# Kernel optimization log

Measured on AMD Instinct MI355X. Metric: run time of the kernel, lower is better.

## Reference

```python
import jax, jax.numpy as jnp
import numpy as np

B, L, D, NHEAD, NLAYERS = 2, 2048, 256, 8, 8
NAMES = ['self', 'cross'] * 4


def setup_inputs() -> dict:
    key = jax.random.key(0)
    ks = jax.random.split(key, 6)
    w_scale = D ** -0.5  # keep activations well-scaled
    return {
        'f0': jax.random.normal(ks[0], (B, L, D), dtype=jnp.float32),
        'f1': jax.random.normal(ks[1], (B, L, D), dtype=jnp.float32),
        'Wq': jax.random.normal(ks[2], (NLAYERS, D, D), dtype=jnp.float32) * w_scale,
        'Wk': jax.random.normal(ks[3], (NLAYERS, D, D), dtype=jnp.float32) * w_scale,
        'Wv': jax.random.normal(ks[4], (NLAYERS, D, D), dtype=jnp.float32) * w_scale,
        'Wo': jax.random.normal(ks[5], (NLAYERS, D, D), dtype=jnp.float32) * w_scale,
    }


def _rope(x, inv_freq):
    # x: (B, L, D); RoPE over the FULL model dim (matches original, mixes heads)
    L_, D_ = x.shape[1], x.shape[2]
    t = jnp.arange(L_, dtype=jnp.float32)
    freqs = t[:, None] * inv_freq[None, :]          # (L, D/2)
    emb = jnp.concatenate([freqs, freqs], axis=-1)  # (L, D)
    x1, x2 = x[..., : D_ // 2], x[..., D_ // 2:]
    rot = jnp.concatenate([-x2, x1], axis=-1)
    return x * jnp.cos(emb) + rot * jnp.sin(emb)


def _attn(x, src, wq, wk, wv, wo, use_rope, inv_freq):
    b, l1, d = x.shape
    l2 = src.shape[1]
    dh = d // NHEAD
    q = x @ wq.T    # torch Linear: x @ W^T
    k = src @ wk.T
    v = src @ wv.T
    if use_rope:
        q = _rope(q, inv_freq)
        k = _rope(k, inv_freq)
    q = q.reshape(b, l1, NHEAD, dh)
    k = k.reshape(b, l2, NHEAD, dh)
    v = v.reshape(b, l2, NHEAD, dh)
    scores = jnp.einsum('bqhd,bkhd->bhqk', q, k) * (dh ** -0.5)
    out = jnp.einsum('bhqk,bkhd->bqhd', jax.nn.softmax(scores, axis=-1), v)
    return out.reshape(b, l1, d) @ wo.T


def reference(f0, f1, Wq, Wk, Wv, Wo):
    d = f0.shape[-1]
    inv_freq = 1.0 / (10000.0 ** (jnp.arange(0, d, 2, dtype=jnp.float32) / d))
    for i, name in enumerate(NAMES):
        if name == 'self':
            f0 = f0 + _attn(f0, f0, Wq[i], Wk[i], Wv[i], Wo[i], True, inv_freq)
            f1 = f1 + _attn(f1, f1, Wq[i], Wk[i], Wv[i], Wo[i], True, inv_freq)
        else:
            # sequential updates: second cross uses the UPDATED f0 (matches torch)
            f0 = f0 + _attn(f0, f1, Wq[i], Wk[i], Wv[i], Wo[i], False, inv_freq)
            f1 = f1 + _attn(f1, f0, Wq[i], Wk[i], Wv[i], Wo[i], False, inv_freq)
    return (f0, f1)
```

## Files before the change

### kernel.cpp

```cpp
#include <hip/hip_runtime.h>

#define BB   2
#define LL   2048
#define DD   256
#define NH   8
#define MM   (BB*LL)
#define NLAYERS 8
#define MMDD ((size_t)MM*DD)

typedef unsigned short ushort_t;
typedef __attribute__((ext_vector_type(8))) short  short8;
typedef __attribute__((ext_vector_type(4))) float  f32x4;
typedef __attribute__((ext_vector_type(4))) unsigned int u32x4;
typedef __attribute__((ext_vector_type(2))) unsigned int u32x2;

#define CSC 0.2550500394f

#define WAITV0 asm volatile("s_waitcnt vmcnt(0)" ::: "memory")
#define WAITV2 asm volatile("s_waitcnt vmcnt(2)" ::: "memory")
#define WAITV4 asm volatile("s_waitcnt vmcnt(4)" ::: "memory")
#define WAITV6 asm volatile("s_waitcnt vmcnt(6)" ::: "memory")
#define WAITLG asm volatile("s_waitcnt lgkmcnt(0)" ::: "memory")
#define BAR()  __builtin_amdgcn_s_barrier()
#define SCHED0 __builtin_amdgcn_sched_barrier(0)

__device__ __forceinline__ f32x4 mfma16(short8 a, short8 b, f32x4 c) {
    return __builtin_amdgcn_mfma_f32_16x16x32_bf16(a, b, c, 0, 0, 0);
}
__device__ __forceinline__ unsigned cvtpk(float lo, float hi) {
    unsigned r;
    asm volatile("v_cvt_pk_bf16_f32 %0, %1, %2" : "=v"(r) : "v"(lo), "v"(hi));
    return r;
}
__device__ __forceinline__ void pl32(unsigned &a, unsigned &b) {
    asm volatile("v_permlane32_swap_b32 %0, %1" : "+v"(a), "+v"(b));
}
__device__ __forceinline__ float bf2f(unsigned short h) {
    return __builtin_bit_cast(float, ((unsigned)h) << 16);
}
__device__ __forceinline__ void gll16(const void* gsrc, void* ldst) {
    __builtin_amdgcn_global_load_lds(
        (const __attribute__((address_space(1))) unsigned int*)gsrc,
        (__attribute__((address_space(3))) unsigned int*)ldst, 16, 0, 0);
}


__global__ __launch_bounds__(256) void setup(const float* __restrict__ f0,
                                             const float* __restrict__ f1,
                                             const float* __restrict__ Wq,
                                             const float* __restrict__ Wk,
                                             const float* __restrict__ Wv,
                                             const float* __restrict__ Wo,
                                             float* __restrict__ F,
                                             ushort_t* __restrict__ Fb,
                                             ushort_t* __restrict__ Wb,
                                             float* __restrict__ tab) {
    int b = blockIdx.x, t = threadIdx.x;
    if (b < 1024) {
        int i = b * 256 + t;
        const float* src = (i < 131072) ? f0 : f1;
        int loc = i & 131071;
        const f32x4* p = (const f32x4*)(src + (size_t)loc * 8);
        f32x4 a = p[0], bb = p[1];
        *(f32x4*)&F[(size_t)i * 8]     = a;
        *(f32x4*)&F[(size_t)i * 8 + 4] = bb;
        u32x4 o = {cvtpk(a.x, a.y), cvtpk(a.z, a.w), cvtpk(bb.x, bb.y), cvtpk(bb.z, bb.w)};
        *(u32x4*)&Fb[(size_t)i * 8] = o;
    } else if (b < 2048) {
        int i = (b - 1024) * 256 + t;
        int reg = i >> 16, loc = i & 65535;
        const float* src = reg == 0 ? Wq : reg == 1 ? Wk : reg == 2 ? Wv : Wo;
        const f32x4* p = (const f32x4*)(src + (size_t)loc * 8);
        f32x4 x = p[0], y = p[1];
        u32x4 o = {cvtpk(x.x, x.y), cvtpk(x.z, x.w), cvtpk(y.x, y.y), cvtpk(y.z, y.w)};
        *(u32x4*)&Wb[(size_t)reg * 524288 + (size_t)loc * 8] = o;
    } else {
        int idx = (b - 2048) * 256 + t;
        int p = idx >> 7, j = idx & 127;
        float inv = __expf(-((float)j / 128.f) * 9.210340371976184f);
        float s, c;
        sincosf((float)p * inv, &s, &c);
        tab[(size_t)p * 256 + j]       = c;
        tab[(size_t)p * 256 + 128 + j] = s;
    }
}

__global__ __launch_bounds__(256) void gemmQK(const ushort_t* __restrict__ X,
                                              const ushort_t* __restrict__ WQ,
                                              const ushort_t* __restrict__ WK,
                                              ushort_t* __restrict__ DQ,
                                              ushort_t* __restrict__ KT,
                                              const float* __restrict__ tab) {
    __shared__ ushort_t Xb[2][4096];
    __shared__ ushort_t WbL[2][4096];
    __shared__ ushort_t WbH[2][4096];
    const int tid = threadIdx.x, ln = tid & 63, w = tid >> 6;
    const int f = blockIdx.x;
    const int xcd = f & 7, u = f >> 3;
    const int bx = u & 3, byg = u >> 2;
    const int mat = bx >> 1, cg = bx & 1;
    const int by = xcd * 16 + byg;
    const int m0 = by * 64, n0 = cg * 64;
    const ushort_t* W = mat ? WK : WQ;

    auto stage = [&](int c, int buf) {
#pragma unroll
        for (int i = 0; i < 2; i++) {
            int sl = (w * 2 + i) * 64 + ln;
            int r = sl >> 3, x = sl & 7;
            int col = c * 64 + ((x ^ (r & 7)) << 3);
            gll16(X + (size_t)(m0 + r) * 256 + col,       &Xb[buf][(w * 2 + i) * 512]);
            gll16(W + (size_t)(n0 + r) * 256 + col,       &WbL[buf][(w * 2 + i) * 512]);
            gll16(W + (size_t)(n0 + 128 + r) * 256 + col, &WbH[buf][(w * 2 + i) * 512]);
        }
    };

    const int ql = ln & 15, gq = ln >> 4;
    const int wm = w >> 1, wn = w & 1;
    f32x4 z4 = {0.f, 0.f, 0.f, 0.f};
    f32x4 accL[2][2] = {{z4, z4}, {z4, z4}};
    f32x4 accH[2][2] = {{z4, z4}, {z4, z4}};

    stage(0, 0);
    stage(1, 1);
#pragma unroll
    for (int c = 0; c < 4; c++) {
        if (c < 3) { WAITV6; } else { WAITV0; }
        BAR(); SCHED0;
        const ushort_t* XL = Xb[c & 1];
        const ushort_t* WL = WbL[c & 1];
        const ushort_t* WH = WbH[c & 1];
        __builtin_amdgcn_s_setprio(1);
#pragma unroll
        for (int ks = 0; ks < 2; ks++) {
            int cc = ks * 4 + gq;
            int r0 = 32 * wm + ql, r1 = r0 + 16;
            int nr0 = 32 * wn + ql, nr1 = nr0 + 16;
            short8 a0 = *(const short8*)&XL[(r0 * 8 + (cc ^ (r0 & 7))) * 8];
            short8 a1 = *(const short8*)&XL[(r1 * 8 + (cc ^ (r1 & 7))) * 8];
            short8 l0 = *(const short8*)&WL[(nr0 * 8 + (cc ^ (nr0 & 7))) * 8];
            short8 l1 = *(const short8*)&WL[(nr1 * 8 + (cc ^ (nr1 & 7))) * 8];
            short8 h0 = *(const short8*)&WH[(nr0 * 8 + (cc ^ (nr0 & 7))) * 8];
            short8 h1 = *(const short8*)&WH[(nr1 * 8 + (cc ^ (nr1 & 7))) * 8];
            accL[0][0] = mfma16(a0, l0, accL[0][0]);
            accL[0][1] = mfma16(a0, l1, accL[0][1]);
            accL[1][0] = mfma16(a1, l0, accL[1][0]);
            accL[1][1] = mfma16(a1, l1, accL[1][1]);
            accH[0][0] = mfma16(a0, h0, accH[0][0]);
            accH[0][1] = mfma16(a0, h1, accH[0][1]);
            accH[1][0] = mfma16(a1, h0, accH[1][0]);
            accH[1][1] = mfma16(a1, h1, accH[1][1]);
        }
        __builtin_amdgcn_s_setprio(0);
        BAR();
        if (c + 2 < 4) stage(c + 2, c & 1);
    }

#pragma unroll
    for (int mf = 0; mf < 2; mf++)
#pragma unroll
        for (int nf = 0; nf < 2; nf++)
#pragma unroll
            for (int r = 0; r < 4; r++) {
                int mg = m0 + 32 * wm + 16 * mf + gq * 4 + r;
                int jl = n0 + 32 * wn + 16 * nf + ql;
                int pos = mg & (LL - 1);
                float a = accL[mf][nf][r], b = accH[mf][nf][r];
                float c = tab[(size_t)pos * 256 + jl];
                float s = tab[(size_t)pos * 256 + 128 + jl];
                float o1 = a * c - b * s;
                float o2 = b * c + a * s;
                if (mat == 0) {
                    o1 *= CSC; o2 *= CSC;
                    DQ[(size_t)mg * 256 + jl]       = (ushort_t)cvtpk(o1, o1);
                    DQ[(size_t)mg * 256 + jl + 128] = (ushort_t)cvtpk(o2, o2);
                } else {
                    int z = mg >> 11, key = mg & 2047;
                    int tt = key >> 6, kk = key & 63;
                    int dh = jl & 31, hA = jl >> 5;
                    size_t base = (size_t)tt * 2048 + (size_t)(dh >> 3) * 512
                                + (size_t)kk * 8 + (dh & 7);
                    KT[(size_t)(z * 8 + hA) * 65536 + base]     = (ushort_t)cvtpk(o1, o1);
                    KT[(size_t)(z * 8 + hA + 4) * 65536 + base] = (ushort_t)cvtpk(o2, o2);
                }
            }
}

template<int NQ, int NK, int NV, int QMODE, int KMODE, int NTY>
__global__ __launch_bounds__(256) void gemm5(const ushort_t* __restrict__ X,
                                             const ushort_t* __restrict__ WQ,
                                             const ushort_t* __restrict__ WK,
                                             const ushort_t* __restrict__ WV,
                                             ushort_t* __restrict__ DQ,
                                             ushort_t* __restrict__ DK,
                                             ushort_t* __restrict__ DVT) {
    constexpr int NTX = NQ + NK + NV;
    __shared__ ushort_t Xb[3][4096];
    __shared__ ushort_t Wb[3][4096];
    const int tid = threadIdx.x, ln = tid & 63, w = tid >> 6;
    const int f = blockIdx.x;
    const int xcd = f & 7, s = f >> 3;
    const int bx = s % NTX, byg = s / NTX;
    const int by = xcd * (NTY / 8) + byg;
    const int m0 = by * 64;

    const ushort_t* W; ushort_t* DH; int n0, mode;
    if (NQ && bx < NQ)           { W = WQ; DH = DQ;  mode = QMODE; n0 = bx * 64; }
    else if (NK && bx < NQ + NK) { W = WK; DH = DK;  mode = KMODE; n0 = (bx - NQ) * 64; }
    else                         { W = WV; DH = DVT; mode = 3; n0 = (bx - NQ - NK) * 64; }

    auto stage = [&](int c, int buf) {
#pragma unroll
        for (int i = 0; i < 2; i++) {
            int sl = (w * 2 + i) * 64 + ln;
            int r = sl >> 3, x = sl & 7;
            int col = c * 64 + ((x ^ (r & 7)) << 3);
            gll16(X + (size_t)(m0 + r) * 256 + col, &Xb[buf][(w * 2 + i) * 512]);
            gll16(W + (size_t)(n0 + r) * 256 + col, &Wb[buf][(w * 2 + i) * 512]);
        }
    };

    const int ql = ln & 15, gq = ln >> 4;
    const int wm = w >> 1, wn = w & 1;
    f32x4 z4 = {0.f, 0.f, 0.f, 0.f};
    f32x4 acc[2][2] = {{z4, z4}, {z4, z4}};

    stage(0, 0);
    stage(1, 1);
#pragma unroll
    for (int c = 0; c < 4; c++) {
        if (c < 3) { WAITV4; } else { WAITV0; }
        BAR(); SCHED0;
        if (c + 2 < 4) stage(c + 2, (c + 2) % 3);
        const ushort_t* XL = Xb[c % 3];
        const ushort_t* WL = Wb[c % 3];
        __builtin_amdgcn_s_setprio(1);
#pragma unroll
        for (int ks = 0; ks < 2; ks++) {
            int cc = ks * 4 + gq;
            int r0 = 32 * wm + ql, r1 = r0 + 16;
            int nr0 = 32 * wn + ql, nr1 = nr0 + 16;
            short8 a0 = *(const short8*)&XL[(r0 * 8 + (cc ^ (r0 & 7))) * 8];
            short8 a1 = *(const short8*)&XL[(r1 * 8 + (cc ^ (r1 & 7))) * 8];
            short8 b0 = *(const short8*)&WL[(nr0 * 8 + (cc ^ (nr0 & 7))) * 8];
            short8 b1 = *(const short8*)&WL[(nr1 * 8 + (cc ^ (nr1 & 7))) * 8];
            acc[0][0] = mfma16(a0, b0, acc[0][0]);
            acc[0][1] = mfma16(a0, b1, acc[0][1]);
            acc[1][0] = mfma16(a1, b0, acc[1][0]);
            acc[1][1] = mfma16(a1, b1, acc[1][1]);
        }
        __builtin_amdgcn_s_setprio(0);
    }

    if (mode == 3) {
        float* scr = (float*)&Xb[0][0];
        __syncthreads();
#pragma unroll
        for (int mf = 0; mf < 2; mf++)
#pragma unroll
            for (int nf = 0; nf < 2; nf++)
#pragma unroll
                for (int r = 0; r < 4; r++) {
                    int nloc = 32 * wn + 16 * nf + ql;
                    int mloc = 32 * wm + 16 * mf + 4 * gq + r;
                    scr[nloc * 65 + mloc] = acc[mf][nf][r];
                }
        __syncthreads();
        int nloc = tid >> 2, mc = (tid & 3) * 16;
        int ng = n0 + nloc, hh = ng >> 5, dh = ng & 31;
        int mg = m0 + mc;
        int z = mg >> 11, key = mg & 2047;
        int tt = key >> 6;
        int ks = (mc >> 5) & 1, J = (mc >> 4) & 1;
        int cA = 4 * ks + 2 * J, cB = cA + 1;
        int swz = dh & 7;
        const float* sc = &scr[nloc * 65 + mc];
        u32x2 q0 = {cvtpk(sc[0], sc[1]),   cvtpk(sc[2], sc[3])};
        u32x2 q1 = {cvtpk(sc[4], sc[5]),   cvtpk(sc[6], sc[7])};
        u32x2 q2 = {cvtpk(sc[8], sc[9]),   cvtpk(sc[10], sc[11])};
        u32x2 q3 = {cvtpk(sc[12], sc[13]), cvtpk(sc[14], sc[15])};
        ushort_t* base = &DVT[(size_t)(z * 8 + hh) * 65536 + (size_t)tt * 2048 + dh * 64];
        *(u32x2*)&base[(cA ^ swz) * 8]     = q0;
        *(u32x2*)&base[(cB ^ swz) * 8]     = q1;
        *(u32x2*)&base[(cA ^ swz) * 8 + 4] = q2;
        *(u32x2*)&base[(cB ^ swz) * 8 + 4] = q3;
    } else {
#pragma unroll
        for (int mf = 0; mf < 2; mf++)
#pragma unroll
            for (int nf = 0; nf < 2; nf++)
#pragma unroll
                for (int r = 0; r < 4; r++) {
                    int mg = m0 + 32 * wm + 16 * mf + gq * 4 + r;
                    int ng = n0 + 32 * wn + 16 * nf + ql;
                    float v = acc[mf][nf][r];
                    if (mode == 2) {
                        DH[(size_t)mg * 256 + ng] = (ushort_t)cvtpk(v, v);
                    } else if (mode == 5) {
                        int zh = (mg >> 11) * 8 + (ng >> 5);
                        size_t off = (size_t)zh * 65536
                                   + (size_t)((mg & 2047) >> 6) * 2048
                                   + (size_t)((ng & 31) >> 3) * 512
                                   + (size_t)(mg & 63) * 8 + (ng & 7);
                        DH[off] = (ushort_t)cvtpk(v, v);
                    } else {
                        float vs = v * CSC;
                        DH[(size_t)mg * 256 + ng] = (ushort_t)cvtpk(vs, vs);
                    }
                }
    }
}

template<int SPLIT, int NTY>
__global__ __launch_bounds__(256) void gemmO(const ushort_t* __restrict__ Opb,
                                             const float* __restrict__ Lp,
                                             const ushort_t* __restrict__ W,
                                             const float* __restrict__ Res,
                                             float* __restrict__ OutF,
                                             ushort_t* __restrict__ OutH,
                                             int mrows) {
    __shared__ ushort_t Xf[64 * 256];
    __shared__ ushort_t Wpb[3][4096];
    const int tid = threadIdx.x, ln = tid & 63, w = tid >> 6;
    const int f = blockIdx.x;
    const int xcd = f & 7, s = f >> 3;
    const int bx = s & 3, byg = s >> 2;
    const int by = xcd * (NTY / 8) + byg;
    const int m0 = by * 64, n0 = bx * 64;

    auto stageW = [&](int c, int buf) {
#pragma unroll
        for (int i = 0; i < 2; i++) {
            int sl = (w * 2 + i) * 64 + ln;
            int r = sl >> 3, x = sl & 7;
            int col = c * 64 + ((x ^ (r & 7)) << 3);
            gll16(W + (size_t)(n0 + r) * 256 + col, &Wpb[buf][(w * 2 + i) * 512]);
        }
    };
    stageW(0, 0);
    stageW(1, 1);

    const int xr = tid >> 2, q = tid & 3, hb = q >> 1;
    float inv[4];
#pragma unroll
    for (int hh = 0; hh < 4; hh++) {
        float l = 0.f;
#pragma unroll
        for (int sp = 0; sp < SPLIT; sp++)
            l += Lp[(size_t)sp * mrows * 8 + (size_t)(m0 + xr) * 8 + 2 * hh + hb];
        inv[hh] = 1.f / l;
    }
#pragma unroll
    for (int p = 0; p < 4; p++) {
        int col = q * 16 + 64 * p;
        f32x4 a0 = {0.f,0.f,0.f,0.f}, a1 = a0, a2 = a0, a3 = a0;
#pragma unroll
        for (int sp = 0; sp < SPLIT; sp++) {
            const ushort_t* src = &Opb[((size_t)sp * mrows + m0 + xr) * 256 + col];
            u32x4 v0 = *(const u32x4*)&src[0];
            u32x4 v1 = *(const u32x4*)&src[8];
            f32x4 b0 = {bf2f(v0.x & 0xffff), bf2f(v0.x >> 16),
                        bf2f(v0.y & 0xffff), bf2f(v0.y >> 16)};
            f32x4 b1 = {bf2f(v0.z & 0xffff), bf2f(v0.z >> 16),
                        bf2f(v0.w & 0xffff), bf2f(v0.w >> 16)};
            f32x4 b2 = {bf2f(v1.x & 0xffff), bf2f(v1.x >> 16),
                        bf2f(v1.y & 0xffff), bf2f(v1.y >> 16)};
            f32x4 b3 = {bf2f(v1.z & 0xffff), bf2f(v1.z >> 16),
                        bf2f(v1.w & 0xffff), bf2f(v1.w >> 16)};
            a0 += b0; a1 += b1; a2 += b2; a3 += b3;
        }
        float iv = inv[p];
        a0 *= iv; a1 *= iv; a2 *= iv; a3 *= iv;
        u32x4 w0 = {cvtpk(a0.x, a0.y), cvtpk(a0.z, a0.w),
                    cvtpk(a1.x, a1.y), cvtpk(a1.z, a1.w)};
        u32x4 w1 = {cvtpk(a2.x, a2.y), cvtpk(a2.z, a2.w),
                    cvtpk(a3.x, a3.y), cvtpk(a3.z, a3.w)};
        int xc0 = q * 2;
        *(u32x4*)&Xf[xr * 256 + p * 64 + ((xc0)     ^ (xr & 7)) * 8] = w0;
        *(u32x4*)&Xf[xr * 256 + p * 64 + ((xc0 + 1) ^ (xr & 7)) * 8] = w1;
    }
    WAITLG;
    BAR(); SCHED0;

    const int ql = ln & 15, gq = ln >> 4;
    const int wm = w >> 1, wn = w & 1;
    f32x4 z4 = {0.f, 0.f, 0.f, 0.f};
    f32x4 acc[2][2] = {{z4, z4}, {z4, z4}};
#pragma unroll
    for (int c = 0; c < 4; c++) {
        if (c < 3) { WAITV2; } else { WAITV0; }
        BAR(); SCHED0;
        if (c + 2 < 4) stageW(c + 2, (c + 2) % 3);
        const ushort_t* WL = Wpb[c % 3];
        __builtin_amdgcn_s_setprio(1);
#pragma unroll
        for (int ks = 0; ks < 2; ks++) {
            int cc = ks * 4 + gq;
            int r0 = 32 * wm + ql, r1 = r0 + 16;
            int nr0 = 32 * wn + ql, nr1 = nr0 + 16;
            short8 a0 = *(const short8*)&Xf[r0 * 256 + c * 64 + (cc ^ (r0 & 7)) * 8];
            short8 a1 = *(const short8*)&Xf[r1 * 256 + c * 64 + (cc ^ (r1 & 7)) * 8];
            short8 b0 = *(const short8*)&WL[(nr0 * 8 + (cc ^ (nr0 & 7))) * 8];
            short8 b1 = *(const short8*)&WL[(nr1 * 8 + (cc ^ (nr1 & 7))) * 8];
            acc[0][0] = mfma16(a0, b0, acc[0][0]);
            acc[0][1] = mfma16(a0, b1, acc[0][1]);
            acc[1][0] = mfma16(a1, b0, acc[1][0]);
            acc[1][1] = mfma16(a1, b1, acc[1][1]);
        }
        __builtin_amdgcn_s_setprio(0);
    }

#pragma unroll
    for (int mf = 0; mf < 2; mf++)
#pragma unroll
        for (int nf = 0; nf < 2; nf++)
#pragma unroll
            for (int r = 0; r < 4; r++) {
                int mg = m0 + 32 * wm + 16 * mf + gq * 4 + r;
                int ng = n0 + 32 * wn + 16 * nf + ql;
                size_t idx = (size_t)mg * 256 + ng;
                float o = Res[idx] + acc[mf][nf][r];
                OutF[idx] = o;
                OutH[idx] = (ushort_t)cvtpk(o, o);
            }
}

template<int SPLIT>
__global__ __launch_bounds__(256, 6) void attn10(const ushort_t* __restrict__ Q,
                                                 const ushort_t* __restrict__ K,
                                                 const ushort_t* __restrict__ Vt,
                                                 ushort_t* __restrict__ Opb,
                                                 float* __restrict__ Lp, int mrows) {
    __shared__ ushort_t K_lds[3][2048];
    __shared__ ushort_t V_lds[3][2048];

    const int tid = threadIdx.x, ln = tid & 63, w = tid >> 6;
    const int ql = ln & 15, gq = ln >> 4;
    const int f = blockIdx.x;
    const int xcd = f & 7, slot = f >> 3;
    const int qb = slot & 15, gg = slot >> 4;
    const int h = xcd;
    const int zz = gg / SPLIT, sp = gg % SPLIT;
    const int t0 = (sp * 32) / SPLIT;
    const int NT = ((sp + 1) * 32) / SPLIT - t0;
    const int q0 = qb * 128 + w * 32;
    const size_t rb = (size_t)zz * 2048;
    const int zh = zz * 8 + h;

    short8 qfA = *(const short8*)&Q[(rb + q0 + ql) * 256 + h * 32 + gq * 8];
    short8 qfB = *(const short8*)&Q[(rb + q0 + 16 + ql) * 256 + h * 32 + gq * 8];

    const ushort_t* kt = K  + (size_t)zh * 65536 + (size_t)t0 * 2048 + tid * 8;
    const ushort_t* vt = Vt + (size_t)zh * 65536 + (size_t)t0 * 2048 + tid * 8;

    gll16(kt,        &K_lds[0][w * 512]);
    gll16(vt,        &V_lds[0][w * 512]);
    gll16(kt + 2048, &K_lds[1][w * 512]);
    gll16(vt + 2048, &V_lds[1][w * 512]);

    const short os = (short)0x3F80;
    const short8 ones = {os, os, os, os, os, os, os, os};
    f32x4 z4 = {0.f, 0.f, 0.f, 0.f};
    f32x4 o0A = z4, o1A = z4, o0B = z4, o1B = z4, laccA = z4, laccB = z4;

    int cur = 0, pre = 2;
    for (int t = 0; t < NT; t++) {
        if (t < NT - 1) { WAITV2; } else { WAITV0; }
        BAR(); SCHED0;
        if (t + 2 < NT) {
            gll16(kt + (size_t)(t + 2) * 2048, &K_lds[pre][w * 512]);
            gll16(vt + (size_t)(t + 2) * 2048, &V_lds[pre][w * 512]);
        }
        const ushort_t* KL = K_lds[cur];
        const ushort_t* VL = V_lds[cur];

        f32x4 stA[4], stB[4];
        __builtin_amdgcn_s_setprio(1);
#pragma unroll
        for (int j = 0; j < 4; j++) {
            short8 kf = *(const short8*)&KL[(gq * 64 + 16 * j + ql) * 8];
            stA[j] = mfma16(kf, qfA, z4);
            stB[j] = mfma16(kf, qfB, z4);
        }
        __builtin_amdgcn_s_setprio(0);
#pragma unroll
        for (int j = 0; j < 4; j++)
#pragma unroll
            for (int r = 0; r < 4; r++) {
                stA[j][r] = __builtin_amdgcn_exp2f(stA[j][r]);
                stB[j][r] = __builtin_amdgcn_exp2f(stB[j][r]);
            }
        unsigned aLo[4], aHi[4], bLo[4], bHi[4];
#pragma unroll
        for (int j = 0; j < 4; j++) {
            aLo[j] = cvtpk(stA[j][0], stA[j][1]);
            aHi[j] = cvtpk(stA[j][2], stA[j][3]);
            bLo[j] = cvtpk(stB[j][0], stB[j][1]);
            bHi[j] = cvtpk(stB[j][2], stB[j][3]);
        }
        pl32(aLo[0], aLo[1]); pl32(aHi[0], aHi[1]);
        pl32(aLo[2], aLo[3]); pl32(aHi[2], aHi[3]);
        pl32(bLo[0], bLo[1]); pl32(bHi[0], bHi[1]);
        pl32(bLo[2], bLo[3]); pl32(bHi[2], bHi[3]);
        u32x4 fA0 = {aLo[0], aHi[0], aLo[1], aHi[1]};
        u32x4 fA1 = {aLo[2], aHi[2], aLo[3], aHi[3]};
        u32x4 fB0 = {bLo[0], bHi[0], bLo[1], bHi[1]};
        u32x4 fB1 = {bLo[2], bHi[2], bLo[3], bHi[3]};
        short8 pfA0 = __builtin_bit_cast(short8, fA0);
        short8 pfA1 = __builtin_bit_cast(short8, fA1);
        short8 pfB0 = __builtin_bit_cast(short8, fB0);
        short8 pfB1 = __builtin_bit_cast(short8, fB1);

        __builtin_amdgcn_s_setprio(1);
#pragma unroll
        for (int ks = 0; ks < 2; ks++) {
            int sw = (4 * ks + gq) ^ (ql & 7);
            short8 vf0 = *(const short8*)&VL[(ql * 8 + sw) * 8];
            short8 vf1 = *(const short8*)&VL[((16 + ql) * 8 + sw) * 8];
            short8 pA = ks ? pfA1 : pfA0;
            short8 pB = ks ? pfB1 : pfB0;
            o0A = mfma16(vf0, pA, o0A);
            o1A = mfma16(vf1, pA, o1A);
            o0B = mfma16(vf0, pB, o0B);
            o1B = mfma16(vf1, pB, o1B);
            laccA = mfma16(ones, pA, laccA);
            laccB = mfma16(ones, pB, laccB);
        }
        __builtin_amdgcn_s_setprio(0);
        cur = (cur == 2) ? 0 : cur + 1;
        pre = (pre == 2) ? 0 : pre + 1;
    }

    size_t rowA = rb + q0 + ql, rowB = rowA + 16;
    ushort_t* obA = Opb + ((size_t)sp * mrows + rowA) * 256 + h * 32;
    ushort_t* obB = Opb + ((size_t)sp * mrows + rowB) * 256 + h * 32;
    u32x2 wA0 = {cvtpk(o0A.x, o0A.y), cvtpk(o0A.z, o0A.w)};
    u32x2 wA1 = {cvtpk(o1A.x, o1A.y), cvtpk(o1A.z, o1A.w)};
    u32x2 wB0 = {cvtpk(o0B.x, o0B.y), cvtpk(o0B.z, o0B.w)};
    u32x2 wB1 = {cvtpk(o1B.x, o1B.y), cvtpk(o1B.z, o1B.w)};
    *(u32x2*)&obA[gq * 4]      = wA0;
    *(u32x2*)&obA[16 + gq * 4] = wA1;
    *(u32x2*)&obB[gq * 4]      = wB0;
    *(u32x2*)&obB[16 + gq * 4] = wB1;
    if (gq == 0) {
        Lp[(size_t)sp * mrows * 8 + rowA * 8 + h] = laccA[0];
        Lp[(size_t)sp * mrows * 8 + rowB * 8 + h] = laccB[0];
    }
}

extern "C" void kernel_launch(void* const* d_in, const int* in_sizes, int n_in,
                              void* d_out, int out_size, void* d_ws, size_t ws_size,
                              hipStream_t stream) {
    const float* f0_in = (const float*)d_in[0];
    const float* f1_in = (const float*)d_in[1];
    const float* Wq = (const float*)d_in[2];
    const float* Wk = (const float*)d_in[3];
    const float* Wv = (const float*)d_in[4];
    const float* Wo = (const float*)d_in[5];

    float* F0 = (float*)d_out;
    float* F1 = F0 + MMDD;

    ushort_t* Fb  = (ushort_t*)d_ws;
    ushort_t* Qb  = Fb  + 2 * MMDD;
    ushort_t* Khb = Qb  + 2 * MMDD;
    ushort_t* Vhb = Khb + 2 * MMDD;
    ushort_t* Wb  = Vhb + 2 * MMDD;
    ushort_t* Opb = Wb  + 2 * MMDD;
    float*    Lpw = (float*)(Opb + 8 * MMDD);
    float*    tab = Lpw + 262144;

    ushort_t* Wqb = Wb;
    ushort_t* Wkb = Wb + (size_t)NLAYERS * 65536;
    ushort_t* Wvb = Wb + (size_t)2 * NLAYERS * 65536;
    ushort_t* Wob = Wb + (size_t)3 * NLAYERS * 65536;

    setup<<<3072, 256, 0, stream>>>(f0_in, f1_in, Wq, Wk, Wv, Wo, F0, Fb, Wb, tab);

    for (int i = 0; i < NLAYERS; i++) {
        const ushort_t* wq = Wqb + (size_t)i * 65536;
        const ushort_t* wk = Wkb + (size_t)i * 65536;
        const ushort_t* wv = Wvb + (size_t)i * 65536;
        const ushort_t* wo = Wob + (size_t)i * 65536;

        if ((i & 1) == 0) {
            gemmQK<<<512, 256, 0, stream>>>(Fb, wq, wk, Qb, Khb, tab);
            gemm5<0, 0, 4, 0, 0, 128><<<512, 256, 0, stream>>>(
                Fb, nullptr, nullptr, wv, nullptr, nullptr, Vhb);
            attn10<3><<<1536, 256, 0, stream>>>(Qb, Khb, Vhb, Opb, Lpw, MM * 2);
            gemmO<3, 128><<<512, 256, 0, stream>>>(Opb, Lpw, wo, F0, F0, Fb, MM * 2);
        } else {
            gemm5<4, 0, 0, 4, 0, 128><<<512, 256, 0, stream>>>(
                Fb, wq, nullptr, nullptr, Qb, nullptr, nullptr);
            for (int s = 0; s < 2; s++) {
                const ushort_t* sb = Fb + (size_t)(1 - s) * MMDD;
                float* xf = s ? F1 : F0;
                ushort_t* xbw = Fb + (size_t)s * MMDD;
                gemm5<0, 4, 4, 0, 5, 64><<<512, 256, 0, stream>>>(
                    sb, nullptr, wk, wv, nullptr, Khb, Vhb);
                attn10<8><<<2048, 256, 0, stream>>>(Qb + (size_t)s * MMDD,
                                                    Khb, Vhb, Opb, Lpw, MM);
                gemmO<8, 64><<<256, 256, 0, stream>>>(Opb, Lpw, wo, xf, xf, xbw, MM);
            }
        }
    }
}
```

Measured before the change: 513.5 us.

## Merge QKV projection launches and slim the attention kernel's pipeline and row-sum

The separate Q/K and V projection kernels are merged into one launch for self layers, and the Q and first K/V projection are merged for cross layers, cutting launch count and tail idle time. The attention kernel goes from triple to double buffering of K/V tiles with a full vmcnt wait, raises its occupancy hint to 8 blocks, and splits self-attention four ways instead of three. The softmax denominator is now summed in scalar registers with a cross-lane shuffle at the end, replacing the extra MFMA against a ones vector. The trade-off is less load/compute overlap in attention, exposing memory latency more, in exchange for higher occupancy and less matrix work.

```diff
diff --git a/kernel.cpp b/kernel.cpp
--- a/kernel.cpp
+++ b/kernel.cpp
@@ -85,17 +85,14 @@
     }
 }
 
-__global__ __launch_bounds__(256) void gemmQK(const ushort_t* __restrict__ X,
-                                              const ushort_t* __restrict__ WQ,
-                                              const ushort_t* __restrict__ WK,
-                                              ushort_t* __restrict__ DQ,
-                                              ushort_t* __restrict__ KT,
-                                              const float* __restrict__ tab) {
-    __shared__ ushort_t Xb[2][4096];
-    __shared__ ushort_t WbL[2][4096];
-    __shared__ ushort_t WbH[2][4096];
+__device__ __forceinline__ void gemmQK_body(int f, ushort_t* lds,
+                                            const ushort_t* __restrict__ X,
+                                            const ushort_t* __restrict__ WQ,
+                                            const ushort_t* __restrict__ WK,
+                                            ushort_t* __restrict__ DQ,
+                                            ushort_t* __restrict__ KT,
+                                            const float* __restrict__ tab) {
     const int tid = threadIdx.x, ln = tid & 63, w = tid >> 6;
-    const int f = blockIdx.x;
     const int xcd = f & 7, u = f >> 3;
     const int bx = u & 3, byg = u >> 2;
     const int mat = bx >> 1, cg = bx & 1;
@@ -109,9 +106,9 @@
             int sl = (w * 2 + i) * 64 + ln;
             int r = sl >> 3, x = sl & 7;
             int col = c * 64 + ((x ^ (r & 7)) << 3);
-            gll16(X + (size_t)(m0 + r) * 256 + col,       &Xb[buf][(w * 2 + i) * 512]);
-            gll16(W + (size_t)(n0 + r) * 256 + col,       &WbL[buf][(w * 2 + i) * 512]);
-            gll16(W + (size_t)(n0 + 128 + r) * 256 + col, &WbH[buf][(w * 2 + i) * 512]);
+            gll16(X + (size_t)(m0 + r) * 256 + col,       &lds[buf * 4096 + (w * 2 + i) * 512]);
+            gll16(W + (size_t)(n0 + r) * 256 + col,       &lds[8192 + buf * 4096 + (w * 2 + i) * 512]);
+            gll16(W + (size_t)(n0 + 128 + r) * 256 + col, &lds[16384 + buf * 4096 + (w * 2 + i) * 512]);
         }
     };
 
@@ -127,9 +124,9 @@
     for (int c = 0; c < 4; c++) {
         if (c < 3) { WAITV6; } else { WAITV0; }
         BAR(); SCHED0;
-        const ushort_t* XL = Xb[c & 1];
-        const ushort_t* WL = WbL[c & 1];
-        const ushort_t* WH = WbH[c & 1];
+        const ushort_t* XL = &lds[(c & 1) * 4096];
+        const ushort_t* WL = &lds[8192 + (c & 1) * 4096];
+        const ushort_t* WH = &lds[16384 + (c & 1) * 4096];
         __builtin_amdgcn_s_setprio(1);
 #pragma unroll
         for (int ks = 0; ks < 2; ks++) {
@@ -187,18 +184,16 @@
 }
 
 template<int NQ, int NK, int NV, int QMODE, int KMODE, int NTY>
-__global__ __launch_bounds__(256) void gemm5(const ushort_t* __restrict__ X,
-                                             const ushort_t* __restrict__ WQ,
-                                             const ushort_t* __restrict__ WK,
-                                             const ushort_t* __restrict__ WV,
-                                             ushort_t* __restrict__ DQ,
-                                             ushort_t* __restrict__ DK,
-                                             ushort_t* __restrict__ DVT) {
+__device__ __forceinline__ void gemm5_body(int f, ushort_t* lds,
+                                           const ushort_t* __restrict__ X,
+                                           const ushort_t* __restrict__ WQ,
+                                           const ushort_t* __restrict__ WK,
+                                           const ushort_t* __restrict__ WV,
+                                           ushort_t* __restrict__ DQ,
+                                           ushort_t* __restrict__ DK,
+                                           ushort_t* __restrict__ DVT) {
     constexpr int NTX = NQ + NK + NV;
-    __shared__ ushort_t Xb[3][4096];
-    __shared__ ushort_t Wb[3][4096];
     const int tid = threadIdx.x, ln = tid & 63, w = tid >> 6;
-    const int f = blockIdx.x;
     const int xcd = f & 7, s = f >> 3;
     const int bx = s % NTX, byg = s / NTX;
     const int by = xcd * (NTY / 8) + byg;
@@ -215,8 +210,8 @@
             int sl = (w * 2 + i) * 64 + ln;
             int r = sl >> 3, x = sl & 7;
             int col = c * 64 + ((x ^ (r & 7)) << 3);
-            gll16(X + (size_t)(m0 + r) * 256 + col, &Xb[buf][(w * 2 + i) * 512]);
-            gll16(W + (size_t)(n0 + r) * 256 + col, &Wb[buf][(w * 2 + i) * 512]);
+            gll16(X + (size_t)(m0 + r) * 256 + col, &lds[buf * 4096 + (w * 2 + i) * 512]);
+            gll16(W + (size_t)(n0 + r) * 256 + col, &lds[12288 + buf * 4096 + (w * 2 + i) * 512]);
         }
     };
 
@@ -232,8 +227,8 @@
         if (c < 3) { WAITV4; } else { WAITV0; }
         BAR(); SCHED0;
         if (c + 2 < 4) stage(c + 2, (c + 2) % 3);
-        const ushort_t* XL = Xb[c % 3];
-        const ushort_t* WL = Wb[c % 3];
+        const ushort_t* XL = &lds[(c % 3) * 4096];
+        const ushort_t* WL = &lds[12288 + (c % 3) * 4096];
         __builtin_amdgcn_s_setprio(1);
 #pragma unroll
         for (int ks = 0; ks < 2; ks++) {
@@ -253,7 +248,7 @@
     }
 
     if (mode == 3) {
-        float* scr = (float*)&Xb[0][0];
+        float* scr = (float*)lds;
         __syncthreads();
 #pragma unroll
         for (int mf = 0; mf < 2; mf++)
@@ -311,6 +306,51 @@
     }
 }
 
+__global__ __launch_bounds__(256) void selfQKV(const ushort_t* __restrict__ Fb,
+                                               const ushort_t* __restrict__ wq,
+                                               const ushort_t* __restrict__ wk,
+                                               const ushort_t* __restrict__ wv,
+                                               ushort_t* __restrict__ Qb,
+                                               ushort_t* __restrict__ Khb,
+                                               ushort_t* __restrict__ Vhb,
+                                               const float* __restrict__ tab) {
+    __shared__ ushort_t lds[24576];
+    int f = blockIdx.x;
+    if (f < 512)
+        gemmQK_body(f, lds, Fb, wq, wk, Qb, Khb, tab);
+    else
+        gemm5_body<0, 0, 4, 0, 0, 128>(f - 512, lds, Fb, nullptr, nullptr, wv,
+                                       nullptr, nullptr, Vhb);
+}
+
+__global__ __launch_bounds__(256) void crossQKV0(const ushort_t* __restrict__ Fb,
+                                                 const ushort_t* __restrict__ wq,
+                                                 const ushort_t* __restrict__ sb,
+                                                 const ushort_t* __restrict__ wk,
+                                                 const ushort_t* __restrict__ wv,
+                                                 ushort_t* __restrict__ Qb,
+                                                 ushort_t* __restrict__ Khb,
+                                                 ushort_t* __restrict__ Vhb) {
+    __shared__ ushort_t lds[24576];
+    int f = blockIdx.x;
+    if (f < 512)
+        gemm5_body<4, 0, 0, 4, 0, 128>(f, lds, Fb, wq, nullptr, nullptr,
+                                       Qb, nullptr, nullptr);
+    else
+        gemm5_body<0, 4, 4, 0, 5, 64>(f - 512, lds, sb, nullptr, wk, wv,
+                                      nullptr, Khb, Vhb);
+}
+
+__global__ __launch_bounds__(256) void gemmKV(const ushort_t* __restrict__ sb,
+                                              const ushort_t* __restrict__ wk,
+                                              const ushort_t* __restrict__ wv,
+                                              ushort_t* __restrict__ Khb,
+                                              ushort_t* __restrict__ Vhb) {
+    __shared__ ushort_t lds[24576];
+    gemm5_body<0, 4, 4, 0, 5, 64>(blockIdx.x, lds, sb, nullptr, wk, wv,
+                                  nullptr, Khb, Vhb);
+}
+
 template<int SPLIT, int NTY>
 __global__ __launch_bounds__(256) void gemmO(const ushort_t* __restrict__ Opb,
                                              const float* __restrict__ Lp,
@@ -426,13 +466,14 @@
 }
 
 template<int SPLIT>
-__global__ __launch_bounds__(256, 6) void attn10(const ushort_t* __restrict__ Q,
+__global__ __launch_bounds__(256, 8) void attn11(const ushort_t* __restrict__ Q,
                                                  const ushort_t* __restrict__ K,
                                                  const ushort_t* __restrict__ Vt,
                                                  ushort_t* __restrict__ Opb,
                                                  float* __restrict__ Lp, int mrows) {
-    __shared__ ushort_t K_lds[3][2048];
-    __shared__ ushort_t V_lds[3][2048];
+    constexpr int NT = 32 / SPLIT;
+    __shared__ ushort_t K_lds[2][2048];
+    __shared__ ushort_t V_lds[2][2048];
 
     const int tid = threadIdx.x, ln = tid & 63, w = tid >> 6;
     const int ql = ln & 15, gq = ln >> 4;
@@ -441,8 +482,7 @@
     const int qb = slot & 15, gg = slot >> 4;
     const int h = xcd;
     const int zz = gg / SPLIT, sp = gg % SPLIT;
-    const int t0 = (sp * 32) / SPLIT;
-    const int NT = ((sp + 1) * 32) / SPLIT - t0;
+    const int t0 = sp * NT;
     const int q0 = qb * 128 + w * 32;
     const size_t rb = (size_t)zz * 2048;
     const int zh = zz * 8 + h;
@@ -453,26 +493,22 @@
     const ushort_t* kt = K  + (size_t)zh * 65536 + (size_t)t0 * 2048 + tid * 8;
     const ushort_t* vt = Vt + (size_t)zh * 65536 + (size_t)t0 * 2048 + tid * 8;
 
-    gll16(kt,        &K_lds[0][w * 512]);
-    gll16(vt,        &V_lds[0][w * 512]);
-    gll16(kt + 2048, &K_lds[1][w * 512]);
-    gll16(vt + 2048, &V_lds[1][w * 512]);
-
-    const short os = (short)0x3F80;
-    const short8 ones = {os, os, os, os, os, os, os, os};
+    gll16(kt, &K_lds[0][w * 512]);
+    gll16(vt, &V_lds[0][w * 512]);
+
     f32x4 z4 = {0.f, 0.f, 0.f, 0.f};
-    f32x4 o0A = z4, o1A = z4, o0B = z4, o1B = z4, laccA = z4, laccB = z4;
-
-    int cur = 0, pre = 2;
+    f32x4 o0A = z4, o1A = z4, o0B = z4, o1B = z4;
+    float lA = 0.f, lB = 0.f;
+
     for (int t = 0; t < NT; t++) {
-        if (t < NT - 1) { WAITV2; } else { WAITV0; }
+        WAITV0;
         BAR(); SCHED0;
-        if (t + 2 < NT) {
-            gll16(kt + (size_t)(t + 2) * 2048, &K_lds[pre][w * 512]);
-            gll16(vt + (size_t)(t + 2) * 2048, &V_lds[pre][w * 512]);
-        }
-        const ushort_t* KL = K_lds[cur];
-        const ushort_t* VL = V_lds[cur];
+        if (t + 1 < NT) {
+            gll16(kt + (size_t)(t + 1) * 2048, &K_lds[(t + 1) & 1][w * 512]);
+            gll16(vt + (size_t)(t + 1) * 2048, &V_lds[(t + 1) & 1][w * 512]);
+        }
+        const ushort_t* KL = K_lds[t & 1];
+        const ushort_t* VL = V_lds[t & 1];
 
         f32x4 stA[4], stB[4];
         __builtin_amdgcn_s_setprio(1);
@@ -490,6 +526,17 @@
                 stA[j][r] = __builtin_amdgcn_exp2f(stA[j][r]);
                 stB[j][r] = __builtin_amdgcn_exp2f(stB[j][r]);
             }
+        float sA = 0.f, sB = 0.f;
+#pragma unroll
+        for (int j = 0; j < 4; j++)
+#pragma unroll
+            for (int r = 0; r < 4; r++) {
+                sA += stA[j][r];
+                sB += stB[j][r];
+            }
+        lA += sA;
+        lB += sB;
+
         unsigned aLo[4], aHi[4], bLo[4], bHi[4];
 #pragma unroll
         for (int j = 0; j < 4; j++) {
@@ -523,13 +570,12 @@
             o1A = mfma16(vf1, pA, o1A);
             o0B = mfma16(vf0, pB, o0B);
             o1B = mfma16(vf1, pB, o1B);
-            laccA = mfma16(ones, pA, laccA);
-            laccB = mfma16(ones, pB, laccB);
         }
         __builtin_amdgcn_s_setprio(0);
-        cur = (cur == 2) ? 0 : cur + 1;
-        pre = (pre == 2) ? 0 : pre + 1;
-    }
+    }
+
+    lA += __shfl_xor(lA, 16); lA += __shfl_xor(lA, 32);
+    lB += __shfl_xor(lB, 16); lB += __shfl_xor(lB, 32);
 
     size_t rowA = rb + q0 + ql, rowB = rowA + 16;
     ushort_t* obA = Opb + ((size_t)sp * mrows + rowA) * 256 + h * 32;
@@ -543,8 +589,8 @@
     *(u32x2*)&obB[gq * 4]      = wB0;
     *(u32x2*)&obB[16 + gq * 4] = wB1;
     if (gq == 0) {
-        Lp[(size_t)sp * mrows * 8 + rowA * 8 + h] = laccA[0];
-        Lp[(size_t)sp * mrows * 8 + rowB * 8 + h] = laccB[0];
+        Lp[(size_t)sp * mrows * 8 + rowA * 8 + h] = lA;
+        Lp[(size_t)sp * mrows * 8 + rowB * 8 + h] = lB;
     }
 }
 
@@ -584,24 +630,18 @@
         const ushort_t* wo = Wob + (size_t)i * 65536;
 
         if ((i & 1) == 0) {
-            gemmQK<<<512, 256, 0, stream>>>(Fb, wq, wk, Qb, Khb, tab);
-            gemm5<0, 0, 4, 0, 0, 128><<<512, 256, 0, stream>>>(
-                Fb, nullptr, nullptr, wv, nullptr, nullptr, Vhb);
-            attn10<3><<<1536, 256, 0, stream>>>(Qb, Khb, Vhb, Opb, Lpw, MM * 2);
-            gemmO<3, 128><<<512, 256, 0, stream>>>(Opb, Lpw, wo, F0, F0, Fb, MM * 2);
+            selfQKV<<<1024, 256, 0, stream>>>(Fb, wq, wk, wv, Qb, Khb, Vhb, tab);
+            attn11<4><<<2048, 256, 0, stream>>>(Qb, Khb, Vhb, Opb, Lpw, MM * 2);
+            gemmO<4, 128><<<512, 256, 0, stream>>>(Opb, Lpw, wo, F0, F0, Fb, MM * 2);
         } else {
-            gemm5<4, 0, 0, 4, 0, 128><<<512, 256, 0, stream>>>(
-                Fb, wq, nullptr, nullptr, Qb, nullptr, nullptr);
-            for (int s = 0; s < 2; s++) {
-                const ushort_t* sb = Fb + (size_t)(1 - s) * MMDD;
-                float* xf = s ? F1 : F0;
-                ushort_t* xbw = Fb + (size_t)s * MMDD;
-                gemm5<0, 4, 4, 0, 5, 64><<<512, 256, 0, stream>>>(
-                    sb, nullptr, wk, wv, nullptr, Khb, Vhb);
-                attn10<8><<<2048, 256, 0, stream>>>(Qb + (size_t)s * MMDD,
-                                                    Khb, Vhb, Opb, Lpw, MM);
-                gemmO<8, 64><<<256, 256, 0, stream>>>(Opb, Lpw, wo, xf, xf, xbw, MM);
-            }
-        }
-    }
-}
+            crossQKV0<<<1024, 256, 0, stream>>>(Fb, wq, Fb + MMDD, wk, wv,
+                                                Qb, Khb, Vhb);
+            attn11<8><<<2048, 256, 0, stream>>>(Qb, Khb, Vhb, Opb, Lpw, MM);
+            gemmO<8, 64><<<256, 256, 0, stream>>>(Opb, Lpw, wo, F0, F0, Fb, MM);
+            gemmKV<<<512, 256, 0, stream>>>(Fb, wk, wv, Khb, Vhb);
+            attn11<8><<<2048, 256, 0, stream>>>(Qb + MMDD, Khb, Vhb, Opb, Lpw, MM);
+            gemmO<8, 64><<<256, 256, 0, stream>>>(Opb, Lpw, wo, F1, F1,
+                                                  Fb + MMDD, MM);
+        }
+    }
+}
```

Result: slower. 923.5 us (+79.8%).
